# Performance work log

Measured on AMD Instinct MI355X. Metric: run time of the kernel, lower is better.

The kernel has to match this reference:

```python
import jax, jax.numpy as jnp
import numpy as np

Nc, Ns, Nt, d_h, BS = 64, 64, 64, 128, 16


def setup_inputs() -> dict:
    key = jax.random.key(0)
    k1, k2, k3, k4, k5 = jax.random.split(key, 5)
    Ac = (jax.random.uniform(k1, (Ns, Nc)) < 0.05).astype(jnp.float32)
    As = (jax.random.uniform(k2, (Ns, Ns)) < 0.05).astype(jnp.float32)
    # AA = As@As@Ac + As@Ac + Ac, then binarize (masked_fill(AA != 0, 1))
    AA = As @ As @ Ac + As @ Ac + Ac
    AA = (AA != 0).astype(jnp.float32)                 # [Ns, Nc]
    AA_mask = jnp.tile(AA, (Nt, Nt))                   # [Ns*Nt, Nc*Nt], == AA.repeat(Nt,Nt) in torch
    GCW = jax.random.normal(k3, (Ns * Nt, Nc * Nt), dtype=jnp.float32)
    GCB = jax.random.normal(k4, (Ns * Nt, d_h), dtype=jnp.float32)
    h = jax.random.normal(k5, (BS, Nc, Nt, d_h), dtype=jnp.float32)
    e = jnp.zeros((1,), jnp.float32)                   # unused in forward (kept for signature parity)
    return {"h": h, "e": e, "AA_mask": AA_mask, "GCW": GCW, "GCB": GCB}


def reference(h, e, AA_mask, GCW, GCB):
    bs = h.shape[0]
    # A = relu(AA.repeat(Nt,Nt) * GCW)  -- structured masked weight [Ns*Nt, Nc*Nt]
    A = jax.nn.relu(AA_mask * GCW)
    # h: [bs, Nc, Nt, d_h] -> [bs, Nt, Nc, d_h] -> [bs, Nt*Nc, d_h]
    x = jnp.transpose(h, (0, 2, 1, 3)).reshape(bs, Nt * Nc, d_h)
    # relu(A @ x + GCB): [bs, Ns*Nt, d_h]
    x = jax.nn.relu(jnp.einsum('ij,bjd->bid', A, x) + GCB)
    # [bs, Nt, Ns, d_h] -> [bs, Ns, Nt, d_h] (final torch reshape is a no-op)
    x = x.reshape(bs, Nt, Ns, d_h)
    x = jnp.transpose(x, (0, 2, 1, 3))
    return x
```

## Files before the change

kernel.cpp:

```cpp
#include <hip/hip_runtime.h>


#define NC 64
#define NS 64
#define NT 64
#define DH 128
#define BATCH 16
#define MDIM 4096
#define KDIM 4096
#define KPAD 4096
#define TM 128
#define TK 64
#define GBM 64
#define GBN 256
#define GBK 64

typedef __attribute__((ext_vector_type(8))) short short8;
typedef __attribute__((ext_vector_type(4))) short short4v;
typedef __attribute__((ext_vector_type(4))) float floatx4;

__device__ __forceinline__ unsigned short f2bf(float f) {
    union { float f; unsigned int i; } v; v.f = f;
    return (unsigned short)((v.i + 0x7fffu + ((v.i >> 16) & 1u)) >> 16);
}
__device__ __forceinline__ void async16(const void* g, void* l) {
    __builtin_amdgcn_global_load_lds(
        (const __attribute__((address_space(1))) void*)g,
        (__attribute__((address_space(3))) void*)l, 16, 0, 0);
}

__global__ __launch_bounds__(256)
void prep(const float* __restrict__ aam, const float* __restrict__ gcw,
          const float* __restrict__ hmat,
          unsigned short* __restrict__ Abf, unsigned short* __restrict__ XT,
          unsigned short* __restrict__ cidx, int* __restrict__ nsb)
{
    const int tid = threadIdx.x;
    if ((int)blockIdx.x < MDIM) {
        const int r  = blockIdx.x;
        const int s  = r >> 6;
        const int tt = r & 63;
        const int i  = tt * 64 + s;
        __shared__ unsigned short scidx[64];
        __shared__ int sns;
        __shared__ unsigned short srow[4096];
        if (tid < 64) {
            float v = aam[(size_t)s * KDIM + tid];
            unsigned long long m = __ballot(v != 0.f);
            int rank = __popcll(m & ((1ull << tid) - 1ull));
            if (v != 0.f) scidx[rank] = (unsigned short)tid;
            if (tid == 0) sns = (int)__popcll(m);
            if (tt == 0) {
                if (v != 0.f) cidx[s * 64 + rank] = (unsigned short)tid;
                if (tid == 0) nsb[s] = (int)__popcll(m);
            }
        }
        const float* gr = gcw + (size_t)i * KDIM;
#pragma unroll
        for (int u = 0; u < 4; ++u) {
            const int idx = u * 1024 + tid * 4;
            floatx4 wv = *(const floatx4*)(gr + idx);
            short4v p;
#pragma unroll
            for (int e = 0; e < 4; ++e) {
                float v = wv[e] > 0.f ? wv[e] : 0.f;
                p[e] = (short)f2bf(v);
            }
            *(short4v*)&srow[idx] = p;
        }
        __syncthreads();
        const int ke = sns * 64;
        for (int kk0 = tid * 8; kk0 < ke; kk0 += 2048) {
            const int c  = (int)scidx[kk0 >> 6];
            const int t0 = kk0 & 63;
            short8 p;
#pragma unroll
            for (int e = 0; e < 8; ++e)
                p[e] = (short)srow[(t0 + e) * 64 + c];
            *(short8*)(Abf + (size_t)r * KPAD + kk0) = p;
        }
    } else {
        const int blk = blockIdx.x - MDIM;
        const int b = blk >> 6;
        const int c = blk & 63;
        __shared__ unsigned short sx[64][136];
        const float* hp = hmat + (((size_t)b * NC + c) * NT) * DH;
#pragma unroll
        for (int u = 0; u < 8; ++u) {
            const int idx = u * 1024 + tid * 4;
            const int t = idx >> 7;
            const int d = idx & 127;
            floatx4 v = *(const floatx4*)(hp + idx);
            short4v p;
#pragma unroll
            for (int e = 0; e < 4; ++e) p[e] = (short)f2bf(v[e]);
            *(short4v*)&sx[t][d] = p;
        }
        __syncthreads();
        const int d  = tid >> 1;
        const int th = (tid & 1) * 32;
        unsigned short* dst = XT + ((size_t)(b * DH + d)) * KPAD + c * 64 + th;
#pragma unroll
        for (int u2 = 0; u2 < 4; ++u2) {
            short8 p;
#pragma unroll
            for (int e = 0; e < 8; ++e)
                p[e] = (short)sx[th + u2 * 8 + e][d];
            *(short8*)(dst + u2 * 8) = p;
        }
    }
}

__global__ __launch_bounds__(256, 2)
void gemm(const unsigned short* __restrict__ Abf,
          const unsigned short* __restrict__ XT,
          const unsigned short* __restrict__ cidx,
          const int* __restrict__ nsb,
          const float* __restrict__ gcb,
          float* __restrict__ out)
{
    __shared__ short lds[2][(GBM + GBN) * GBK];

    const int tid = threadIdx.x;
    const int bid = blockIdx.x;
    const int np = bid & 7;
    const int s  = bid >> 3;
    const int n0 = np * GBN;

    const int lane = tid & 63;
    const int w    = tid >> 6;
    const int wn   = w * 64;
    const int l15  = lane & 15;
    const int q    = lane >> 4;
    const int srow = lane >> 3;
    const int swz  = ((lane & 7) ^ srow) << 3;

    const int nt = nsb[s];
    const int cl = (int)cidx[s * 64 + lane];

    const unsigned short* Ab = Abf + (size_t)(s * 64) * KPAD + swz;
    const unsigned short* Xb = XT  + (size_t)n0 * KPAD + swz;

    floatx4 acc[4][4];
#pragma unroll
    for (int mi = 0; mi < 4; ++mi)
#pragma unroll
        for (int ni = 0; ni < 4; ++ni)
            acc[mi][ni] = (floatx4){0.f, 0.f, 0.f, 0.f};

    auto stage = [&](int t, int b) {
        short* dst = lds[b];
        const int c = __shfl(cl, t);
        const size_t ka = (size_t)t * GBK;
        const size_t kx = (size_t)c * GBK;
        async16(Ab + (size_t)(w * 8 + srow) * KPAD + ka,       dst + (w * 8) * GBK);
        async16(Ab + (size_t)((w + 4) * 8 + srow) * KPAD + ka, dst + ((w + 4) * 8) * GBK);
#pragma unroll
        for (int g = 0; g < 8; ++g) {
            const int rr = w * 64 + g * 8;
            async16(Xb + (size_t)(rr + srow) * KPAD + kx, dst + (GBM + rr) * GBK);
        }
    };

    auto compute = [&](int b) {
        const short* sA = lds[b];
        const short* sX = lds[b] + GBM * GBK;
#pragma unroll
        for (int h2 = 0; h2 < 2; ++h2) {
            const int co = ((h2 * 4 + q) ^ (l15 & 7)) << 3;
            short8 af[4], xf[4];
#pragma unroll
            for (int mi = 0; mi < 4; ++mi)
                af[mi] = *(const short8*)&sA[(mi * 16 + l15) * GBK + co];
#pragma unroll
            for (int ni = 0; ni < 4; ++ni)
                xf[ni] = *(const short8*)&sX[(wn + ni * 16 + l15) * GBK + co];
            __builtin_amdgcn_s_setprio(1);
#pragma unroll
            for (int mi = 0; mi < 4; ++mi)
#pragma unroll
                for (int ni = 0; ni < 4; ++ni)
                    acc[mi][ni] = __builtin_amdgcn_mfma_f32_16x16x32_bf16(
                        af[mi], xf[ni], acc[mi][ni], 0, 0, 0);
            __builtin_amdgcn_s_setprio(0);
        }
    };

    if (nt > 0) stage(0, 0);
    if (nt > 1) stage(1, 1);
    for (int t = 0; t < nt - 1; ++t) {
        asm volatile("s_waitcnt vmcnt(10)" ::: "memory");
        __builtin_amdgcn_s_barrier();
        compute(t & 1);
        __builtin_amdgcn_s_barrier();
        if (t + 2 < nt) stage(t + 2, t & 1);
    }
    if (nt > 0) {
        asm volatile("s_waitcnt vmcnt(0)" ::: "memory");
        __builtin_amdgcn_s_barrier();
        compute((nt - 1) & 1);
    }

#pragma unroll
    for (int mi = 0; mi < 4; ++mi) {
        const int tt0 = mi * 16 + q * 4;
#pragma unroll
        for (int ni = 0; ni < 4; ++ni) {
            const int n  = n0 + wn + ni * 16 + l15;
            const int bb = n >> 7;
            const int d  = n & 127;
#pragma unroll
            for (int r = 0; r < 4; ++r) {
                const int tt = tt0 + r;
                const int i  = tt * 64 + s;
                float v = acc[mi][ni][r] + gcb[(size_t)i * DH + d];
                v = v > 0.f ? v : 0.f;
                out[(((size_t)bb * NS + s) * NT + tt) * DH + d] = v;
            }
        }
    }
}

#define APAD 40
#define XPAD 20
__global__ __launch_bounds__(256, 2)
void gcn_fused(const float* __restrict__ hmat, const float* __restrict__ aam,
               const float* __restrict__ gcw, const float* __restrict__ gcb,
               float* __restrict__ out)
{
    __shared__ short sA[TM * APAD];
    __shared__ unsigned int sX[DH * XPAD];
    const int tid = threadIdx.x;
    const int bid = blockIdx.x;
    const int mp  = (bid & 7) * 4 + (bid >> 7);
    const int b   = (bid >> 3) & 15;
    const int i0  = mp * TM;
    const int lane = tid & 63;
    const int wm = ((tid >> 6) >> 1) * 64;
    const int wn = ((tid >> 6) & 1) * 64;
    const int l15 = lane & 15;
    const int q   = lane >> 4;
    floatx4 acc[4][4];
#pragma unroll
    for (int mi = 0; mi < 4; ++mi)
#pragma unroll
        for (int ni = 0; ni < 4; ++ni) acc[mi][ni] = (floatx4){0.f,0.f,0.f,0.f};
    const int ar = tid >> 2, ac = (tid & 3) << 3;
    const int kp = tid >> 4, dg = (tid & 15) << 3;
    const int wkey = (tid & 3) << 2;
    for (int k0 = 0; k0 < KDIM; k0 += 32) {
        const size_t ga0 = (size_t)(i0 + ar) * KDIM + (k0 + ac);
        const size_t ga1 = ga0 + (size_t)64 * KDIM;
        floatx4 aa0a = *(const floatx4*)(aam + ga0), aa0b = *(const floatx4*)(aam + ga0 + 4);
        floatx4 ww0a = *(const floatx4*)(gcw + ga0), ww0b = *(const floatx4*)(gcw + ga0 + 4);
        floatx4 aa1a = *(const floatx4*)(aam + ga1), aa1b = *(const floatx4*)(aam + ga1 + 4);
        floatx4 ww1a = *(const floatx4*)(gcw + ga1), ww1b = *(const floatx4*)(gcw + ga1 + 4);
        const int jj = k0 + 2 * kp, tt = jj >> 6, cc = jj & 63;
        const size_t gx0 = ((size_t)(b * NC + cc) * NT + tt) * DH + dg;
        const size_t gx1 = gx0 + (size_t)NT * DH;
        floatx4 x0a = *(const floatx4*)(hmat + gx0), x0b = *(const floatx4*)(hmat + gx0 + 4);
        floatx4 x1a = *(const floatx4*)(hmat + gx1), x1b = *(const floatx4*)(hmat + gx1 + 4);
        __syncthreads();
        short8 p0, p1;
#pragma unroll
        for (int e = 0; e < 4; ++e) {
            float v0 = aa0a[e]*ww0a[e]; v0 = v0>0.f?v0:0.f;
            float v1 = aa0b[e]*ww0b[e]; v1 = v1>0.f?v1:0.f;
            float v2 = aa1a[e]*ww1a[e]; v2 = v2>0.f?v2:0.f;
            float v3 = aa1b[e]*ww1b[e]; v3 = v3>0.f?v3:0.f;
            p0[e] = (short)f2bf(v0); p0[e+4] = (short)f2bf(v1);
            p1[e] = (short)f2bf(v2); p1[e+4] = (short)f2bf(v3);
        }
        *(short8*)&sA[ar * APAD + ac] = p0;
        *(short8*)&sA[(ar + 64) * APAD + ac] = p1;
#pragma unroll
        for (int e = 0; e < 4; ++e) {
            unsigned int pka = (unsigned int)f2bf(x0a[e]) | ((unsigned int)f2bf(x1a[e]) << 16);
            unsigned int pkb = (unsigned int)f2bf(x0b[e]) | ((unsigned int)f2bf(x1b[e]) << 16);
            sX[(dg + e) * XPAD + (kp ^ wkey)] = pka;
            sX[(dg + e + 4) * XPAD + (kp ^ wkey)] = pkb;
        }
        __syncthreads();
        short8 afrag[4], bfrag[4];
#pragma unroll
        for (int mi = 0; mi < 4; ++mi)
            afrag[mi] = *(const short8*)&sA[(wm + mi * 16 + l15) * APAD + q * 8];
#pragma unroll
        for (int ni = 0; ni < 4; ++ni) {
            const int row = wn + ni * 16 + l15;
            const int col = (q * 4) ^ (((row >> 3) & 3) << 2);
            bfrag[ni] = *(const short8*)(sX + row * XPAD + col);
        }
#pragma unroll
        for (int mi = 0; mi < 4; ++mi)
#pragma unroll
            for (int ni = 0; ni < 4; ++ni)
                acc[mi][ni] = __builtin_amdgcn_mfma_f32_16x16x32_bf16(
                    afrag[mi], bfrag[ni], acc[mi][ni], 0, 0, 0);
    }
#pragma unroll
    for (int mi = 0; mi < 4; ++mi) {
        const int ibase = i0 + wm + mi * 16 + q * 4;
#pragma unroll
        for (int ni = 0; ni < 4; ++ni) {
            const int d = wn + ni * 16 + l15;
#pragma unroll
            for (int r = 0; r < 4; ++r) {
                const int i = ibase + r;
                float v = acc[mi][ni][r] + gcb[(size_t)i * DH + d];
                v = v > 0.f ? v : 0.f;
                out[(((size_t)b * NS + (i & 63)) * NT + (i >> 6)) * DH + d] = v;
            }
        }
    }
}

extern "C" void kernel_launch(void* const* d_in, const int* in_sizes, int n_in,
                              void* d_out, int out_size, void* d_ws, size_t ws_size,
                              hipStream_t stream) {
    const float* h   = (const float*)d_in[0];
    const float* aam = (const float*)d_in[2];
    const float* gcw = (const float*)d_in[3];
    const float* gcb = (const float*)d_in[4];
    float* out = (float*)d_out;

    const size_t A_BYTES   = (size_t)MDIM * KPAD * 2;
    const size_t XT_BYTES  = (size_t)BATCH * DH * KPAD * 2;
    const size_t IDX_BYTES = 64 * 64 * 2;
    const size_t NS_BYTES  = 64 * 4;

    if (ws_size >= A_BYTES + XT_BYTES + IDX_BYTES + NS_BYTES) {
        unsigned short* Abf = (unsigned short*)d_ws;
        unsigned short* XTp = (unsigned short*)((char*)d_ws + A_BYTES);
        unsigned short* cid = (unsigned short*)((char*)d_ws + A_BYTES + XT_BYTES);
        int* nsb            = (int*)((char*)d_ws + A_BYTES + XT_BYTES + IDX_BYTES);
        prep<<<dim3(MDIM + BATCH * NT), 256, 0, stream>>>(aam, gcw, h, Abf, XTp, cid, nsb);
        gemm<<<dim3(64 * 8), 256, 0, stream>>>(Abf, XTp, cid, nsb, gcb, out);
    } else {
        gcn_fused<<<dim3((MDIM / TM) * BATCH), 256, 0, stream>>>(h, aam, gcw, gcb, out);
    }
}
```

Measured before the change: 229.3 us.

## Triple-buffer GEMM LDS pipeline and gather GCW directly in prep

The GEMM main loop moves from a two-stage to a three-stage LDS ring buffer, issuing loads three tiles ahead with matching vmcnt waits, to hide more global-load latency. LDS use grows to about 120KB per block, which may cut occupancy below the two blocks per CU requested in launch bounds. Separately, the prep kernel no longer converts the whole GCW row into LDS. It now reads only the needed strided columns straight from global memory, doing less work for sparse rows but with uncoalesced accesses.

```diff
diff --git a/kernel.cpp b/kernel.cpp
--- a/kernel.cpp
+++ b/kernel.cpp
@@ -43,7 +43,6 @@
         const int i  = tt * 64 + s;
         __shared__ unsigned short scidx[64];
         __shared__ int sns;
-        __shared__ unsigned short srow[4096];
         if (tid < 64) {
             float v = aam[(size_t)s * KDIM + tid];
             unsigned long long m = __ballot(v != 0.f);
@@ -55,28 +54,19 @@
                 if (tid == 0) nsb[s] = (int)__popcll(m);
             }
         }
-        const float* gr = gcw + (size_t)i * KDIM;
-#pragma unroll
-        for (int u = 0; u < 4; ++u) {
-            const int idx = u * 1024 + tid * 4;
-            floatx4 wv = *(const floatx4*)(gr + idx);
-            short4v p;
-#pragma unroll
-            for (int e = 0; e < 4; ++e) {
-                float v = wv[e] > 0.f ? wv[e] : 0.f;
-                p[e] = (short)f2bf(v);
-            }
-            *(short4v*)&srow[idx] = p;
-        }
         __syncthreads();
         const int ke = sns * 64;
+        const float* gr = gcw + (size_t)i * KDIM;
         for (int kk0 = tid * 8; kk0 < ke; kk0 += 2048) {
             const int c  = (int)scidx[kk0 >> 6];
             const int t0 = kk0 & 63;
             short8 p;
 #pragma unroll
-            for (int e = 0; e < 8; ++e)
-                p[e] = (short)srow[(t0 + e) * 64 + c];
+            for (int e = 0; e < 8; ++e) {
+                float v = gr[(t0 + e) * 64 + c];
+                v = v > 0.f ? v : 0.f;
+                p[e] = (short)f2bf(v);
+            }
             *(short8*)(Abf + (size_t)r * KPAD + kk0) = p;
         }
     } else {
@@ -119,7 +109,7 @@
           const float* __restrict__ gcb,
           float* __restrict__ out)
 {
-    __shared__ short lds[2][(GBM + GBN) * GBK];
+    __shared__ short lds[3][(GBM + GBN) * GBK];
 
     const int tid = threadIdx.x;
     const int bid = blockIdx.x;
@@ -188,17 +178,17 @@
 
     if (nt > 0) stage(0, 0);
     if (nt > 1) stage(1, 1);
-    for (int t = 0; t < nt - 1; ++t) {
-        asm volatile("s_waitcnt vmcnt(10)" ::: "memory");
+    if (nt > 2) stage(2, 2);
+    for (int t = 0; t < nt; ++t) {
+        const int rem = nt - 1 - t;
+        if (rem >= 2)      asm volatile("s_waitcnt vmcnt(20)" ::: "memory");
+        else if (rem == 1) asm volatile("s_waitcnt vmcnt(10)" ::: "memory");
+        else               asm volatile("s_waitcnt vmcnt(0)"  ::: "memory");
         __builtin_amdgcn_s_barrier();
-        compute(t & 1);
+        const int b = t % 3;
+        compute(b);
         __builtin_amdgcn_s_barrier();
-        if (t + 2 < nt) stage(t + 2, t & 1);
-    }
-    if (nt > 0) {
-        asm volatile("s_waitcnt vmcnt(0)" ::: "memory");
-        __builtin_amdgcn_s_barrier();
-        compute((nt - 1) & 1);
+        if (t + 3 < nt) stage(t + 3, b);
     }
 
 #pragma unroll
```

Result: slower. 254.5 us (+11.0%).
